# Optimization experiments

Measured on AMD Instinct MI355X. Metric: run time of the kernel, lower is better.

Reference implementation:

```python
import jax, jax.numpy as jnp
import numpy as np

NN = 262144        # total nodes = 4096 graphs * 64 nodes
EN = 524288        # directed edges
IN_DIM = 32
H = 128
PROP_STEPS = 3


def setup_inputs() -> dict:
    key = jax.random.key(0)
    ks = jax.random.split(key, 16)
    s = lambda d: 1.0 / np.sqrt(d)
    x = jax.random.normal(ks[0], (NN, IN_DIM), dtype=jnp.float32)
    # edges: random within each 64-node graph block would be most faithful; random
    # over NN is the same access pattern workload-wise. Use per-graph-local edges.
    src = jax.random.randint(ks[1], (EN,), 0, NN, dtype=jnp.int64)
    dst = jax.random.randint(ks[2], (EN,), 0, NN, dtype=jnp.int64)
    edge_index = jnp.stack([src, dst], axis=0)
    return {
        "x": x,
        "edge_index": edge_index,
        "W_in": jax.random.normal(ks[3], (IN_DIM, H), jnp.float32) * s(IN_DIM),
        "b_in": jnp.zeros((H,), jnp.float32),
        "W_e1": jax.random.normal(ks[4], (H, H), jnp.float32) * s(H),
        "b_e1": jnp.zeros((H,), jnp.float32),
        "W_e2": jax.random.normal(ks[5], (H, H), jnp.float32) * s(H),
        "b_e2": jnp.zeros((H,), jnp.float32),
        "W_ih": jax.random.normal(ks[6], (H, 3 * H), jnp.float32) * s(H),
        "b_ih": jnp.zeros((3 * H,), jnp.float32),
        "W_hh": jax.random.normal(ks[7], (H, 3 * H), jnp.float32) * s(H),
        "b_hh": jnp.zeros((3 * H,), jnp.float32),
        "W_out": jax.random.normal(ks[8], (H, 1), jnp.float32) * s(H),
        "b_out": jnp.zeros((1,), jnp.float32),
    }


def reference(x, edge_index, W_in, b_in, W_e1, b_e1, W_e2, b_e2,
              W_ih, b_ih, W_hh, b_hh, W_out, b_out):
    in_node, out_node = edge_index[0], edge_index[1]
    nn = x.shape[0]
    # input MLP: Linear + tanh
    h = jnp.tanh(x @ W_in + b_in)                         # [NN, H]
    for _ in range(PROP_STEPS):
        # unified edge MLP (hidden tanh + linear out), applied per node then gathered
        m = jnp.tanh(h @ W_e1 + b_e1) @ W_e2 + b_e2       # [NN, H]
        msg = m[in_node]                                  # [EN, H] gather
        ssum = jax.ops.segment_sum(msg, out_node, num_segments=nn)
        cnt = jax.ops.segment_sum(jnp.ones((msg.shape[0],), msg.dtype),
                                  out_node, num_segments=nn)
        m_agg = ssum / jnp.maximum(cnt, 1.0)[:, None]     # scatter_mean, [NN, H]
        # GRU cell update: input = m_agg, hidden = h (torch GRUCell math)
        gi = m_agg @ W_ih + b_ih                          # [NN, 3H]
        gh = h @ W_hh + b_hh                              # [NN, 3H]
        i_r, i_z, i_n = jnp.split(gi, 3, axis=-1)
        h_r, h_z, h_n = jnp.split(gh, 3, axis=-1)
        r = jax.nn.sigmoid(i_r + h_r)
        z = jax.nn.sigmoid(i_z + h_z)
        n = jnp.tanh(i_n + r * h_n)
        h = (1.0 - z) * n + z * h
    # unified output head: single Linear
    return h @ W_out + b_out                              # [NN, 1]
```

## Files before the change

kernel.cpp:

```cpp
#include <hip/hip_runtime.h>

#define NN 262144
#define EN 524288
#define HD 128
#define IND 32

#define NT64  (NN/64)
#define GRID_E 768
#define NT128 (NN/128)
#define GRID_G 256

typedef __attribute__((ext_vector_type(8))) short s16x8;
typedef __attribute__((ext_vector_type(4))) float f32x4;
typedef unsigned short u16;
typedef unsigned int u32;

#define MFMA(a,b,c) __builtin_amdgcn_mfma_f32_16x16x32_bf16(a,b,c,0,0,0)
#define SWZ(p) ((p) ^ ((((p)>>8)&7)<<4))

typedef __attribute__((address_space(1))) void gas_void;
typedef __attribute__((address_space(3))) void las_void;
__device__ __forceinline__ void gload16(const void* g, void* l){
  __builtin_amdgcn_global_load_lds((gas_void*)g, (las_void*)l, 16, 0, 0);
}

__device__ __forceinline__ u16 f2b(float f){
  u32 u = __builtin_bit_cast(u32, f);
  u = (u + 0x7fffu + ((u >> 16) & 1u)) >> 16;
  return (u16)u;
}
__device__ __forceinline__ float b2f(u32 lo16){ return __builtin_bit_cast(float, lo16 << 16); }
__device__ __forceinline__ float rcpf_(float x){ return __builtin_amdgcn_rcpf(x); }
__device__ __forceinline__ float fsig(float x){ return rcpf_(1.f + __expf(-x)); }
__device__ __forceinline__ float ftanh(float x){ return 1.f - 2.f*rcpf_(1.f + __expf(2.f*x)); }

__global__ __launch_bounds__(256) void k_w2bt(const float* __restrict__ W, u16* __restrict__ Wt, int K, int N){
  int idx = blockIdx.x*256 + threadIdx.x;
  if (idx >= K*N) return;
  int n = idx / K, k = idx - n*K;
  Wt[idx] = f2b(W[k*N + n]);
}

__global__ void k_eflag(const int* __restrict__ ei, int* __restrict__ flag){
  int v = ei[threadIdx.x*2 + 1];
  unsigned long long b = __ballot(v != 0);
  if (threadIdx.x == 0) flag[0] = (b == 0ULL) ? 1 : 0;
}
__device__ __forceinline__ int eget(const int* ei, int f, int which, int e){
  return f ? ei[(which*EN + e)*2] : ei[which*EN + e];
}

__global__ __launch_bounds__(256) void k_count(const int* __restrict__ ei, const int* __restrict__ flag, int* __restrict__ cnt){
  int e = blockIdx.x*256 + threadIdx.x;
  if (e < EN) atomicAdd(&cnt[eget(ei, flag[0], 1, e)], 1);
}
__global__ __launch_bounds__(256) void k_scan1(const int* __restrict__ cnt, int* __restrict__ excl, int* __restrict__ bsum){
  __shared__ int ws[4];
  int i = blockIdx.x*256 + threadIdx.x;
  int v = cnt[i];
  int ln = threadIdx.x & 63;
  int x = v;
  #pragma unroll
  for (int d=1; d<64; d<<=1){ int y = __shfl_up(x, d); if (ln >= d) x += y; }
  if (ln == 63) ws[threadIdx.x>>6] = x;
  __syncthreads();
  int wpre = 0;
  for (int j=0; j<(threadIdx.x>>6); ++j) wpre += ws[j];
  excl[i] = wpre + x - v;
  if (threadIdx.x == 255) bsum[blockIdx.x] = wpre + x;
}
__global__ __launch_bounds__(1024) void k_scan2(int* __restrict__ bsum){
  __shared__ int ws[16];
  int i = threadIdx.x;
  int v = bsum[i];
  int ln = i & 63;
  int x = v;
  #pragma unroll
  for (int d=1; d<64; d<<=1){ int y = __shfl_up(x, d); if (ln >= d) x += y; }
  if (ln == 63) ws[i>>6] = x;
  __syncthreads();
  int wpre = 0;
  for (int j=0; j<(i>>6); ++j) wpre += ws[j];
  bsum[i] = wpre + x - v;
}
__global__ __launch_bounds__(256) void k_scan3(const int* __restrict__ excl, const int* __restrict__ bsum, int* __restrict__ rp, int* __restrict__ cur){
  int i = blockIdx.x*256 + threadIdx.x;
  int v = excl[i] + bsum[blockIdx.x];
  rp[i] = v; cur[i] = v;
  if (i == 0) rp[NN] = EN;
}
__global__ __launch_bounds__(256) void k_fill(const int* __restrict__ ei, const int* __restrict__ flag, int* __restrict__ cur, int* __restrict__ cx){
  int e = blockIdx.x*256 + threadIdx.x;
  if (e >= EN) return;
  int f = flag[0];
  int p = atomicAdd(&cur[eget(ei, f, 1, e)], 1);
  cx[p] = eget(ei, f, 0, e);
}

__global__ __launch_bounds__(256) void k_input(const float* __restrict__ x, const u16* __restrict__ wt, const float* __restrict__ bias, u16* __restrict__ h){
  const int wv = threadIdx.x >> 6, ln = threadIdx.x & 63;
  const int l15 = ln & 15, lg = ln >> 4;
  const int base = blockIdx.x*128 + wv*32;
  s16x8 a[2];
  #pragma unroll
  for (int rt=0; rt<2; ++rt){
    const float* xp = x + (base + rt*16 + l15)*IND + lg*8;
    float4 v0 = *reinterpret_cast<const float4*>(xp);
    float4 v1 = *reinterpret_cast<const float4*>(xp + 4);
    s16x8 t;
    t[0]=(short)f2b(v0.x); t[1]=(short)f2b(v0.y); t[2]=(short)f2b(v0.z); t[3]=(short)f2b(v0.w);
    t[4]=(short)f2b(v1.x); t[5]=(short)f2b(v1.y); t[6]=(short)f2b(v1.z); t[7]=(short)f2b(v1.w);
    a[rt] = t;
  }
  #pragma unroll
  for (int cg=0; cg<8; ++cg){
    const int col = cg*16 + l15;
    s16x8 bf = *reinterpret_cast<const s16x8*>(wt + col*IND + lg*8);
    float bb = bias[col];
    f32x4 acc0 = {bb,bb,bb,bb}, acc1 = {bb,bb,bb,bb};
    acc0 = MFMA(a[0], bf, acc0);
    acc1 = MFMA(a[1], bf, acc1);
    #pragma unroll
    for (int r=0; r<4; ++r){
      h[(base + lg*4 + r)*HD + col]      = f2b(ftanh(acc0[r]));
      h[(base + 16 + lg*4 + r)*HD + col] = f2b(ftanh(acc1[r]));
    }
  }
}

__global__ __launch_bounds__(512) void k_edge(const u16* __restrict__ h, const u16* __restrict__ wt1, const float* __restrict__ b1,
                                              const u16* __restrict__ wt2, const float* __restrict__ b2, u16* __restrict__ m){
  extern __shared__ __align__(1024) unsigned char lds[];
  const int tid = threadIdx.x, wv = tid >> 6, ln = tid & 63;
  const int l15 = ln & 15, lg = ln >> 4;
  const int col = wv*16 + l15;

  s16x8 B1[4], B2[4];
  #pragma unroll
  for (int kk=0; kk<4; ++kk){
    const int ko = kk*32 + lg*8;
    B1[kk] = *reinterpret_cast<const s16x8*>(wt1 + (size_t)col*HD + ko);
    B2[kk] = *reinterpret_cast<const s16x8*>(wt2 + (size_t)col*HD + ko);
  }
  const float b1s = b1[col], b2s = b2[col];

  {
    const unsigned char* hg = (const unsigned char*)h + (size_t)blockIdx.x*64*256;
    #pragma unroll
    for (int i=0; i<2; ++i){
      int c = wv*2 + i;
      int p = c*1024 + ln*16;
      gload16(hg + SWZ(p), lds + c*1024);
    }
  }
  __syncthreads();

  unsigned char* tl = lds + 32768;
  int t = 0;
  #pragma unroll 1
  for (int tt = blockIdx.x; tt < NT64; tt += GRID_E, ++t){
    if (tt + GRID_E < NT64){
      const unsigned char* hg = (const unsigned char*)h + (size_t)(tt+GRID_E)*64*256;
      unsigned char* dst = lds + ((t+1)&1)*16384;
      #pragma unroll
      for (int i=0; i<2; ++i){
        int c = wv*2 + i;
        int p = c*1024 + ln*16;
        gload16(hg + SWZ(p), dst + c*1024);
      }
    }
    const unsigned char* hl = lds + (t&1)*16384;
    for (int rt=0; rt<4; ++rt){
      s16x8 a[4];
      #pragma unroll
      for (int kk=0; kk<4; ++kk){
        int row = rt*16 + l15;
        int p = row*256 + (((kk*4+lg) ^ (row&7))<<4);
        a[kk] = *reinterpret_cast<const s16x8*>(hl + p);
      }
      f32x4 acc = {b1s,b1s,b1s,b1s};
      __builtin_amdgcn_s_setprio(1);
      #pragma unroll
      for (int kk=0; kk<4; ++kk) acc = MFMA(a[kk], B1[kk], acc);
      __builtin_amdgcn_s_setprio(0);
      #pragma unroll
      for (int r=0; r<4; ++r){
        int row = rt*16 + lg*4 + r;
        int tb = row*256 + ((((col*2)>>4) ^ (row&7))<<4) + ((col&7)*2);
        *reinterpret_cast<u16*>(tl + tb) = f2b(ftanh(acc[r]));
      }
    }
    __syncthreads();
    for (int rt=0; rt<4; ++rt){
      s16x8 a[4];
      #pragma unroll
      for (int kk=0; kk<4; ++kk){
        int row = rt*16 + l15;
        int p = row*256 + (((kk*4+lg) ^ (row&7))<<4);
        a[kk] = *reinterpret_cast<const s16x8*>(tl + p);
      }
      f32x4 acc = {b2s,b2s,b2s,b2s};
      __builtin_amdgcn_s_setprio(1);
      #pragma unroll
      for (int kk=0; kk<4; ++kk) acc = MFMA(a[kk], B2[kk], acc);
      __builtin_amdgcn_s_setprio(0);
      #pragma unroll
      for (int r=0; r<4; ++r){
        int row = rt*16 + lg*4 + r;
        m[(size_t)(tt*64+row)*HD + col] = f2b(acc[r]);
      }
    }
    __syncthreads();
  }
}

__global__ __launch_bounds__(256) void k_agg(const u16* __restrict__ m, const int* __restrict__ rp, const int* __restrict__ cx, u16* __restrict__ magg){
  const int sub = threadIdx.x >> 5, l32 = threadIdx.x & 31;
  const int n = blockIdx.x*8 + sub;
  int s0 = rp[n], s1 = rp[n+1];
  float a0=0.f, a1=0.f, a2=0.f, a3=0.f;
  int p = s0;
  for (; p + 2 <= s1; p += 2){
    int na = cx[p], nb = cx[p+1];
    uint2 va = *reinterpret_cast<const uint2*>(m + (size_t)na*HD + l32*4);
    uint2 vb = *reinterpret_cast<const uint2*>(m + (size_t)nb*HD + l32*4);
    a0 += b2f(va.x & 0xffffu) + b2f(vb.x & 0xffffu);
    a1 += b2f(va.x >> 16)     + b2f(vb.x >> 16);
    a2 += b2f(va.y & 0xffffu) + b2f(vb.y & 0xffffu);
    a3 += b2f(va.y >> 16)     + b2f(vb.y >> 16);
  }
  if (p < s1){
    int na = cx[p];
    uint2 va = *reinterpret_cast<const uint2*>(m + (size_t)na*HD + l32*4);
    a0 += b2f(va.x & 0xffffu); a1 += b2f(va.x >> 16);
    a2 += b2f(va.y & 0xffffu); a3 += b2f(va.y >> 16);
  }
  int deg = s1 - s0;
  float inv = rcpf_((float)(deg > 0 ? deg : 1));
  uint2 o;
  o.x = (u32)f2b(a0*inv) | ((u32)f2b(a1*inv) << 16);
  o.y = (u32)f2b(a2*inv) | ((u32)f2b(a3*inv) << 16);
  *reinterpret_cast<uint2*>(magg + (size_t)n*HD + l32*4) = o;
}

__global__ __launch_bounds__(512) void k_gru(const u16* __restrict__ magg, u16* __restrict__ h,
    const u16* __restrict__ wtih, const float* __restrict__ bih,
    const u16* __restrict__ wthh, const float* __restrict__ bhh){
  extern __shared__ __align__(1024) unsigned char lds[];
  const int tid = threadIdx.x, wv = tid >> 6, ln = tid & 63;
  const int l15 = ln & 15, lg = ln >> 4;
  const int col = wv*16 + l15;
  const int ce = col & ~1;

  s16x8 B[6][4];
  #pragma unroll
  for (int kk=0; kk<4; ++kk){
    const int ko = kk*32 + lg*8;
    B[0][kk] = *reinterpret_cast<const s16x8*>(wtih + (size_t)(col       )*HD + ko);
    B[1][kk] = *reinterpret_cast<const s16x8*>(wtih + (size_t)(col +   HD)*HD + ko);
    B[2][kk] = *reinterpret_cast<const s16x8*>(wtih + (size_t)(col + 2*HD)*HD + ko);
    B[3][kk] = *reinterpret_cast<const s16x8*>(wthh + (size_t)(col       )*HD + ko);
    B[4][kk] = *reinterpret_cast<const s16x8*>(wthh + (size_t)(col +   HD)*HD + ko);
    B[5][kk] = *reinterpret_cast<const s16x8*>(wthh + (size_t)(col + 2*HD)*HD + ko);
  }
  const float brz = bih[col] + bhh[col];
  const float bzz = bih[col+HD] + bhh[col+HD];
  const float bin_ = bih[col+2*HD], bhn_ = bhh[col+2*HD];

  {
    const unsigned char* mg = (const unsigned char*)magg + (size_t)blockIdx.x*128*256;
    const unsigned char* hg = (const unsigned char*)h    + (size_t)blockIdx.x*128*256;
    #pragma unroll
    for (int i=0; i<8; ++i){
      int c = wv*8 + i;
      int p = (c & 31)*1024 + ln*16;
      gload16((c < 32 ? mg : hg) + SWZ(p), lds + c*1024);
    }
  }
  __syncthreads();

#define LOADA(rt, amg, ahh, hld) { \
    const int row_ = (rt)*16 + l15; \
    _Pragma("unroll") \
    for (int kk=0; kk<4; ++kk){ \
      int p_ = row_*256 + (((kk*4+lg) ^ (row_&7))<<4); \
      amg[kk] = *reinterpret_cast<const s16x8*>(mgl + p_); \
      ahh[kk] = *reinterpret_cast<const s16x8*>(hl + p_); } \
    _Pragma("unroll") \
    for (int r_=0; r_<4; ++r_){ \
      int hrow_ = (rt)*16 + lg*4 + r_; \
      int hb_ = hrow_*256 + ((((ce*2)>>4) ^ (hrow_&7))<<4) + ((ce&7)*2); \
      hld[r_] = *reinterpret_cast<const u32*>(hl + hb_); } }

#define MFMAS(amg, ahh, aR, aZ, aN, aH) { \
    aR = (f32x4){brz,brz,brz,brz}; aZ = (f32x4){bzz,bzz,bzz,bzz}; \
    aN = (f32x4){bin_,bin_,bin_,bin_}; aH = (f32x4){bhn_,bhn_,bhn_,bhn_}; \
    __builtin_amdgcn_s_setprio(1); \
    _Pragma("unroll") \
    for (int kk=0; kk<4; ++kk){ \
      aR = MFMA(amg[kk], B[0][kk], aR); \
      aZ = MFMA(amg[kk], B[1][kk], aZ); \
      aN = MFMA(amg[kk], B[2][kk], aN); \
      aH = MFMA(ahh[kk], B[5][kk], aH); \
      aR = MFMA(ahh[kk], B[3][kk], aR); \
      aZ = MFMA(ahh[kk], B[4][kk], aZ); } \
    __builtin_amdgcn_s_setprio(0); }

#define EPI(rt, aR, aZ, aN, aH, hld) { \
    _Pragma("unroll") \
    for (int r_=0; r_<4; ++r_){ \
      int row_ = (rt)*16 + lg*4 + r_; \
      float hold_ = __builtin_bit_cast(float, (col&1) ? (hld[r_] & 0xffff0000u) : (hld[r_] << 16)); \
      float rg_ = fsig(aR[r_]); \
      float zg_ = fsig(aZ[r_]); \
      float ng_ = ftanh(aN[r_] + rg_*aH[r_]); \
      h[(size_t)(tt*128+row_)*HD + col] = f2b(ng_ + zg_*(hold_ - ng_)); } }

  int t = 0;
  #pragma unroll 1
  for (int tt = blockIdx.x; tt < NT128; tt += GRID_G, ++t){
    if (tt + GRID_G < NT128){
      const unsigned char* mg = (const unsigned char*)magg + (size_t)(tt+GRID_G)*128*256;
      const unsigned char* hg = (const unsigned char*)h    + (size_t)(tt+GRID_G)*128*256;
      unsigned char* dst = lds + ((t+1)&1)*65536;
      #pragma unroll
      for (int i=0; i<8; ++i){
        int c = wv*8 + i;
        int p = (c & 31)*1024 + ln*16;
        gload16((c < 32 ? mg : hg) + SWZ(p), dst + c*1024);
      }
    }
    const unsigned char* mgl = lds + (t&1)*65536;
    const unsigned char* hl  = mgl + 32768;

    s16x8 amgA[4], ahhA[4], amgB[4], ahhB[4];
    u32 hldA[4], hldB[4];
    f32x4 rA, zA, nA, hA, rB, zB, nB, hB;

    LOADA(0, amgA, ahhA, hldA); MFMAS(amgA, ahhA, rA, zA, nA, hA);
    LOADA(1, amgB, ahhB, hldB); MFMAS(amgB, ahhB, rB, zB, nB, hB); EPI(0, rA, zA, nA, hA, hldA);
    LOADA(2, amgA, ahhA, hldA); MFMAS(amgA, ahhA, rA, zA, nA, hA); EPI(1, rB, zB, nB, hB, hldB);
    LOADA(3, amgB, ahhB, hldB); MFMAS(amgB, ahhB, rB, zB, nB, hB); EPI(2, rA, zA, nA, hA, hldA);
    LOADA(4, amgA, ahhA, hldA); MFMAS(amgA, ahhA, rA, zA, nA, hA); EPI(3, rB, zB, nB, hB, hldB);
    LOADA(5, amgB, ahhB, hldB); MFMAS(amgB, ahhB, rB, zB, nB, hB); EPI(4, rA, zA, nA, hA, hldA);
    LOADA(6, amgA, ahhA, hldA); MFMAS(amgA, ahhA, rA, zA, nA, hA); EPI(5, rB, zB, nB, hB, hldB);
    LOADA(7, amgB, ahhB, hldB); MFMAS(amgB, ahhB, rB, zB, nB, hB); EPI(6, rA, zA, nA, hA, hldA);
    EPI(7, rB, zB, nB, hB, hldB);

    __syncthreads();
  }
#undef LOADA
#undef MFMAS
#undef EPI
}

__global__ __launch_bounds__(256) void k_out(const u16* __restrict__ h, const float* __restrict__ wo, const float* __restrict__ bo, float* __restrict__ out){
  const int wv = threadIdx.x >> 6, ln = threadIdx.x & 63;
  const int n = (blockIdx.x*4 + wv)*4 + (ln >> 4);
  const int kc = (ln & 15)*8;
  uint4 v = *reinterpret_cast<const uint4*>(h + n*HD + kc);
  float4 w0 = *reinterpret_cast<const float4*>(wo + kc);
  float4 w1 = *reinterpret_cast<const float4*>(wo + kc + 4);
  float s = b2f(v.x & 0xffffu)*w0.x + b2f(v.x >> 16)*w0.y + b2f(v.y & 0xffffu)*w0.z + b2f(v.y >> 16)*w0.w
          + b2f(v.z & 0xffffu)*w1.x + b2f(v.z >> 16)*w1.y + b2f(v.w & 0xffffu)*w1.z + b2f(v.w >> 16)*w1.w;
  #pragma unroll
  for (int d=1; d<16; d<<=1) s += __shfl_xor(s, d, 16);
  if ((ln & 15) == 0) out[n] = s + bo[0];
}

#define AL256(x) ((((size_t)(x)) + 255) & ~(size_t)255)
static const size_t SZ_STATE = (size_t)NN*HD*2;
static const size_t OFF_H    = 0;
static const size_t OFF_M    = OFF_H + SZ_STATE;
static const size_t OFF_MAGG = OFF_M + SZ_STATE;
static const size_t OFF_RP   = OFF_MAGG + SZ_STATE;
static const size_t OFF_CUR  = OFF_RP + AL256((size_t)(NN+1)*4);
static const size_t OFF_CNT  = OFF_CUR + (size_t)NN*4;
static const size_t OFF_EXCL = OFF_CNT + (size_t)NN*4;
static const size_t OFF_BSUM = OFF_EXCL + (size_t)NN*4;
static const size_t OFF_CX   = OFF_BSUM + AL256(1024*4);
static const size_t OFF_FLAG = OFF_CX + (size_t)EN*4;
static const size_t OFF_WTIN = OFF_FLAG + 256;
static const size_t OFF_WTE1 = OFF_WTIN + AL256((size_t)IND*HD*2);
static const size_t OFF_WTE2 = OFF_WTE1 + AL256((size_t)HD*HD*2);
static const size_t OFF_WTIH = OFF_WTE2 + AL256((size_t)HD*HD*2);
static const size_t OFF_WTHH = OFF_WTIH + AL256((size_t)HD*3*HD*2);

extern "C" void kernel_launch(void* const* d_in, const int* in_sizes, int n_in,
                              void* d_out, int out_size, void* d_ws, size_t ws_size,
                              hipStream_t stream){
  const float* x    = (const float*)d_in[0];
  const int*   ei   = (const int*)d_in[1];
  const float* W_in = (const float*)d_in[2];  const float* b_in = (const float*)d_in[3];
  const float* W_e1 = (const float*)d_in[4];  const float* b_e1 = (const float*)d_in[5];
  const float* W_e2 = (const float*)d_in[6];  const float* b_e2 = (const float*)d_in[7];
  const float* W_ih = (const float*)d_in[8];  const float* b_ih = (const float*)d_in[9];
  const float* W_hh = (const float*)d_in[10]; const float* b_hh = (const float*)d_in[11];
  const float* W_out= (const float*)d_in[12]; const float* b_out= (const float*)d_in[13];
  float* out = (float*)d_out;

  char* ws = (char*)d_ws;
  u16* h    = (u16*)(ws + OFF_H);
  u16* m    = (u16*)(ws + OFF_M);
  u16* magg = (u16*)(ws + OFF_MAGG);
  int* rp   = (int*)(ws + OFF_RP);
  int* cur  = (int*)(ws + OFF_CUR);
  int* cnt  = (int*)(ws + OFF_CNT);
  int* excl = (int*)(ws + OFF_EXCL);
  int* bsum = (int*)(ws + OFF_BSUM);
  int* cx   = (int*)(ws + OFF_CX);
  int* flag = (int*)(ws + OFF_FLAG);
  u16* wtin = (u16*)(ws + OFF_WTIN);
  u16* wte1 = (u16*)(ws + OFF_WTE1);
  u16* wte2 = (u16*)(ws + OFF_WTE2);
  u16* wtih = (u16*)(ws + OFF_WTIH);
  u16* wthh = (u16*)(ws + OFF_WTHH);

  hipFuncSetAttribute((const void*)k_edge, hipFuncAttributeMaxDynamicSharedMemorySize, 49152);
  hipFuncSetAttribute((const void*)k_gru,  hipFuncAttributeMaxDynamicSharedMemorySize, 131072);

  hipMemsetAsync(cnt, 0, (size_t)NN*4, stream);

  k_w2bt<<<(IND*HD + 255)/256, 256, 0, stream>>>(W_in, wtin, IND, HD);
  k_w2bt<<<(HD*HD + 255)/256, 256, 0, stream>>>(W_e1, wte1, HD, HD);
  k_w2bt<<<(HD*HD + 255)/256, 256, 0, stream>>>(W_e2, wte2, HD, HD);
  k_w2bt<<<(HD*3*HD + 255)/256, 256, 0, stream>>>(W_ih, wtih, HD, 3*HD);
  k_w2bt<<<(HD*3*HD + 255)/256, 256, 0, stream>>>(W_hh, wthh, HD, 3*HD);

  k_eflag<<<1, 64, 0, stream>>>(ei, flag);
  k_count<<<EN/256, 256, 0, stream>>>(ei, flag, cnt);
  k_scan1<<<NN/256, 256, 0, stream>>>(cnt, excl, bsum);
  k_scan2<<<1, 1024, 0, stream>>>(bsum);
  k_scan3<<<NN/256, 256, 0, stream>>>(excl, bsum, rp, cur);
  k_fill<<<EN/256, 256, 0, stream>>>(ei, flag, cur, cx);

  k_input<<<NN/128, 256, 0, stream>>>(x, wtin, b_in, h);

  for (int it=0; it<3; ++it){
    k_edge<<<GRID_E, 512, 49152, stream>>>(h, wte1, b_e1, wte2, b_e2, m);
    k_agg<<<NN/8, 256, 0, stream>>>(m, rp, cx, magg);
    k_gru<<<GRID_G, 512, 131072, stream>>>(magg, h, wtih, b_ih, wthh, b_hh);
  }
  k_out<<<NN/16, 256, 0, stream>>>(h, W_out, b_out, out);
}
```

Baseline: 534.4 us.

## Split GRU tiles into column halves with ping-pong hidden-state buffers

The GRU kernel moves from 512-thread blocks over 128-row tiles to 256-thread blocks, two per CU, each handling 64 rows and half of the output columns. This halves LDS use per block and gives finer-grained work distribution. Because two blocks now read the same rows of h, the hidden state is ping-ponged between two buffers, and the message buffer reuses the output slot. The cost is that each block loads the full magg and h rows, so input traffic into LDS doubles. Activations also switch to exp2-based forms with fma, and stores use precomputed pointers.

```diff
diff --git a/kernel.cpp b/kernel.cpp
--- a/kernel.cpp
+++ b/kernel.cpp
@@ -7,8 +7,8 @@
 
 #define NT64  (NN/64)
 #define GRID_E 768
-#define NT128 (NN/128)
-#define GRID_G 256
+#define NJOB  (NT64*2)
+#define GRID_G2 512
 
 typedef __attribute__((ext_vector_type(8))) short s16x8;
 typedef __attribute__((ext_vector_type(4))) float f32x4;
@@ -29,10 +29,14 @@
   u = (u + 0x7fffu + ((u >> 16) & 1u)) >> 16;
   return (u16)u;
 }
+__device__ __forceinline__ u32 cvtpk(float lo, float hi){
+  return (u32)f2b(lo) | ((u32)f2b(hi) << 16);
+}
 __device__ __forceinline__ float b2f(u32 lo16){ return __builtin_bit_cast(float, lo16 << 16); }
 __device__ __forceinline__ float rcpf_(float x){ return __builtin_amdgcn_rcpf(x); }
-__device__ __forceinline__ float fsig(float x){ return rcpf_(1.f + __expf(-x)); }
-__device__ __forceinline__ float ftanh(float x){ return 1.f - 2.f*rcpf_(1.f + __expf(2.f*x)); }
+__device__ __forceinline__ float exp2_(float x){ return __builtin_amdgcn_exp2f(x); }
+__device__ __forceinline__ float fsig(float x){ return rcpf_(1.f + exp2_(x * -1.442695041f)); }
+__device__ __forceinline__ float ftanh(float x){ return fmaf(-2.f, rcpf_(1.f + exp2_(x * 2.885390082f)), 1.f); }
 
 __global__ __launch_bounds__(256) void k_w2bt(const float* __restrict__ W, u16* __restrict__ Wt, int K, int N){
   int idx = blockIdx.x*256 + threadIdx.x;
@@ -122,8 +126,8 @@
     acc1 = MFMA(a[1], bf, acc1);
     #pragma unroll
     for (int r=0; r<4; ++r){
-      h[(base + lg*4 + r)*HD + col]      = f2b(ftanh(acc0[r]));
-      h[(base + 16 + lg*4 + r)*HD + col] = f2b(ftanh(acc1[r]));
+      h[(size_t)(base + lg*4 + r)*HD + col]      = f2b(ftanh(acc0[r]));
+      h[(size_t)(base + 16 + lg*4 + r)*HD + col] = f2b(ftanh(acc1[r]));
     }
   }
 }
@@ -204,11 +208,11 @@
       #pragma unroll
       for (int kk=0; kk<4; ++kk) acc = MFMA(a[kk], B2[kk], acc);
       __builtin_amdgcn_s_setprio(0);
-      #pragma unroll
-      for (int r=0; r<4; ++r){
-        int row = rt*16 + lg*4 + r;
-        m[(size_t)(tt*64+row)*HD + col] = f2b(acc[r]);
-      }
+      u16* mp = m + (size_t)(tt*64 + rt*16 + lg*4)*HD + col;
+      mp[0]    = f2b(acc[0]);
+      mp[HD]   = f2b(acc[1]);
+      mp[2*HD] = f2b(acc[2]);
+      mp[3*HD] = f2b(acc[3]);
     }
     __syncthreads();
   }
@@ -238,18 +242,19 @@
   int deg = s1 - s0;
   float inv = rcpf_((float)(deg > 0 ? deg : 1));
   uint2 o;
-  o.x = (u32)f2b(a0*inv) | ((u32)f2b(a1*inv) << 16);
-  o.y = (u32)f2b(a2*inv) | ((u32)f2b(a3*inv) << 16);
+  o.x = cvtpk(a0*inv, a1*inv);
+  o.y = cvtpk(a2*inv, a3*inv);
   *reinterpret_cast<uint2*>(magg + (size_t)n*HD + l32*4) = o;
 }
 
-__global__ __launch_bounds__(512) void k_gru(const u16* __restrict__ magg, u16* __restrict__ h,
+__global__ __launch_bounds__(256, 2) void k_gru(const u16* __restrict__ magg, const u16* __restrict__ hin, u16* __restrict__ hout,
     const u16* __restrict__ wtih, const float* __restrict__ bih,
     const u16* __restrict__ wthh, const float* __restrict__ bhh){
   extern __shared__ __align__(1024) unsigned char lds[];
   const int tid = threadIdx.x, wv = tid >> 6, ln = tid & 63;
   const int l15 = ln & 15, lg = ln >> 4;
-  const int col = wv*16 + l15;
+  const int ch = blockIdx.x & 1;
+  const int col = ch*64 + wv*16 + l15;
   const int ce = col & ~1;
 
   s16x8 B[6][4];
@@ -268,13 +273,14 @@
   const float bin_ = bih[col+2*HD], bhn_ = bhh[col+2*HD];
 
   {
-    const unsigned char* mg = (const unsigned char*)magg + (size_t)blockIdx.x*128*256;
-    const unsigned char* hg = (const unsigned char*)h    + (size_t)blockIdx.x*128*256;
+    const size_t rbase = (size_t)(blockIdx.x >> 1)*64*256;
+    const unsigned char* mg = (const unsigned char*)magg + rbase;
+    const unsigned char* hg = (const unsigned char*)hin  + rbase;
     #pragma unroll
     for (int i=0; i<8; ++i){
       int c = wv*8 + i;
-      int p = (c & 31)*1024 + ln*16;
-      gload16((c < 32 ? mg : hg) + SWZ(p), lds + c*1024);
+      int p = (c & 15)*1024 + ln*16;
+      gload16((c < 16 ? mg : hg) + SWZ(p), lds + c*1024);
     }
   }
   __syncthreads();
@@ -307,31 +313,33 @@
     __builtin_amdgcn_s_setprio(0); }
 
 #define EPI(rt, aR, aZ, aN, aH, hld) { \
+    u16* hp_ = hout + (size_t)(rowt*64 + (rt)*16 + lg*4)*HD + col; \
     _Pragma("unroll") \
     for (int r_=0; r_<4; ++r_){ \
-      int row_ = (rt)*16 + lg*4 + r_; \
       float hold_ = __builtin_bit_cast(float, (col&1) ? (hld[r_] & 0xffff0000u) : (hld[r_] << 16)); \
       float rg_ = fsig(aR[r_]); \
       float zg_ = fsig(aZ[r_]); \
       float ng_ = ftanh(aN[r_] + rg_*aH[r_]); \
-      h[(size_t)(tt*128+row_)*HD + col] = f2b(ng_ + zg_*(hold_ - ng_)); } }
+      hp_[r_*HD] = f2b(ng_ + zg_*(hold_ - ng_)); } }
 
   int t = 0;
   #pragma unroll 1
-  for (int tt = blockIdx.x; tt < NT128; tt += GRID_G, ++t){
-    if (tt + GRID_G < NT128){
-      const unsigned char* mg = (const unsigned char*)magg + (size_t)(tt+GRID_G)*128*256;
-      const unsigned char* hg = (const unsigned char*)h    + (size_t)(tt+GRID_G)*128*256;
-      unsigned char* dst = lds + ((t+1)&1)*65536;
+  for (int job = blockIdx.x; job < NJOB; job += GRID_G2, ++t){
+    const int rowt = job >> 1;
+    if (job + GRID_G2 < NJOB){
+      const size_t rbase = (size_t)((job + GRID_G2) >> 1)*64*256;
+      const unsigned char* mg = (const unsigned char*)magg + rbase;
+      const unsigned char* hg = (const unsigned char*)hin  + rbase;
+      unsigned char* dst = lds + ((t+1)&1)*32768;
       #pragma unroll
       for (int i=0; i<8; ++i){
         int c = wv*8 + i;
-        int p = (c & 31)*1024 + ln*16;
-        gload16((c < 32 ? mg : hg) + SWZ(p), dst + c*1024);
+        int p = (c & 15)*1024 + ln*16;
+        gload16((c < 16 ? mg : hg) + SWZ(p), dst + c*1024);
       }
     }
-    const unsigned char* mgl = lds + (t&1)*65536;
-    const unsigned char* hl  = mgl + 32768;
+    const unsigned char* mgl = lds + (t&1)*32768;
+    const unsigned char* hl  = mgl + 16384;
 
     s16x8 amgA[4], ahhA[4], amgB[4], ahhB[4];
     u32 hldA[4], hldB[4];
@@ -341,11 +349,7 @@
     LOADA(1, amgB, ahhB, hldB); MFMAS(amgB, ahhB, rB, zB, nB, hB); EPI(0, rA, zA, nA, hA, hldA);
     LOADA(2, amgA, ahhA, hldA); MFMAS(amgA, ahhA, rA, zA, nA, hA); EPI(1, rB, zB, nB, hB, hldB);
     LOADA(3, amgB, ahhB, hldB); MFMAS(amgB, ahhB, rB, zB, nB, hB); EPI(2, rA, zA, nA, hA, hldA);
-    LOADA(4, amgA, ahhA, hldA); MFMAS(amgA, ahhA, rA, zA, nA, hA); EPI(3, rB, zB, nB, hB, hldB);
-    LOADA(5, amgB, ahhB, hldB); MFMAS(amgB, ahhB, rB, zB, nB, hB); EPI(4, rA, zA, nA, hA, hldA);
-    LOADA(6, amgA, ahhA, hldA); MFMAS(amgA, ahhA, rA, zA, nA, hA); EPI(5, rB, zB, nB, hB, hldB);
-    LOADA(7, amgB, ahhB, hldB); MFMAS(amgB, ahhB, rB, zB, nB, hB); EPI(6, rA, zA, nA, hA, hldA);
-    EPI(7, rB, zB, nB, hB, hldB);
+    EPI(3, rB, zB, nB, hB, hldB);
 
     __syncthreads();
   }
@@ -358,7 +362,7 @@
   const int wv = threadIdx.x >> 6, ln = threadIdx.x & 63;
   const int n = (blockIdx.x*4 + wv)*4 + (ln >> 4);
   const int kc = (ln & 15)*8;
-  uint4 v = *reinterpret_cast<const uint4*>(h + n*HD + kc);
+  uint4 v = *reinterpret_cast<const uint4*>(h + (size_t)n*HD + kc);
   float4 w0 = *reinterpret_cast<const float4*>(wo + kc);
   float4 w1 = *reinterpret_cast<const float4*>(wo + kc + 4);
   float s = b2f(v.x & 0xffffu)*w0.x + b2f(v.x >> 16)*w0.y + b2f(v.y & 0xffffu)*w0.z + b2f(v.y >> 16)*w0.w
@@ -370,9 +374,9 @@
 
 #define AL256(x) ((((size_t)(x)) + 255) & ~(size_t)255)
 static const size_t SZ_STATE = (size_t)NN*HD*2;
-static const size_t OFF_H    = 0;
-static const size_t OFF_M    = OFF_H + SZ_STATE;
-static const size_t OFF_MAGG = OFF_M + SZ_STATE;
+static const size_t OFF_HA   = 0;
+static const size_t OFF_HB   = OFF_HA + SZ_STATE;
+static const size_t OFF_MAGG = OFF_HB + SZ_STATE;
 static const size_t OFF_RP   = OFF_MAGG + SZ_STATE;
 static const size_t OFF_CUR  = OFF_RP + AL256((size_t)(NN+1)*4);
 static const size_t OFF_CNT  = OFF_CUR + (size_t)NN*4;
@@ -400,8 +404,8 @@
   float* out = (float*)d_out;
 
   char* ws = (char*)d_ws;
-  u16* h    = (u16*)(ws + OFF_H);
-  u16* m    = (u16*)(ws + OFF_M);
+  u16* hA   = (u16*)(ws + OFF_HA);
+  u16* hB   = (u16*)(ws + OFF_HB);
   u16* magg = (u16*)(ws + OFF_MAGG);
   int* rp   = (int*)(ws + OFF_RP);
   int* cur  = (int*)(ws + OFF_CUR);
@@ -417,7 +421,7 @@
   u16* wthh = (u16*)(ws + OFF_WTHH);
 
   hipFuncSetAttribute((const void*)k_edge, hipFuncAttributeMaxDynamicSharedMemorySize, 49152);
-  hipFuncSetAttribute((const void*)k_gru,  hipFuncAttributeMaxDynamicSharedMemorySize, 131072);
+  hipFuncSetAttribute((const void*)k_gru,  hipFuncAttributeMaxDynamicSharedMemorySize, 65536);
 
   hipMemsetAsync(cnt, 0, (size_t)NN*4, stream);
 
@@ -434,12 +438,14 @@
   k_scan3<<<NN/256, 256, 0, stream>>>(excl, bsum, rp, cur);
   k_fill<<<EN/256, 256, 0, stream>>>(ei, flag, cur, cx);
 
-  k_input<<<NN/128, 256, 0, stream>>>(x, wtin, b_in, h);
+  k_input<<<NN/128, 256, 0, stream>>>(x, wtin, b_in, hA);
 
   for (int it=0; it<3; ++it){
-    k_edge<<<GRID_E, 512, 49152, stream>>>(h, wte1, b_e1, wte2, b_e2, m);
-    k_agg<<<NN/8, 256, 0, stream>>>(m, rp, cx, magg);
-    k_gru<<<GRID_G, 512, 131072, stream>>>(magg, h, wtih, b_ih, wthh, b_hh);
-  }
-  k_out<<<NN/16, 256, 0, stream>>>(h, W_out, b_out, out);
-}
+    u16* hin  = (it & 1) ? hB : hA;
+    u16* hout = (it & 1) ? hA : hB;
+    k_edge<<<GRID_E, 512, 49152, stream>>>(hin, wte1, b_e1, wte2, b_e2, hout);
+    k_agg<<<NN/8, 256, 0, stream>>>(hout, rp, cx, magg);
+    k_gru<<<GRID_G2, 256, 65536, stream>>>(magg, hin, hout, wtih, b_ih, wthh, b_hh);
+  }
+  k_out<<<NN/16, 256, 0, stream>>>(hB, W_out, b_out, out);
+}
```

Result: no change. 527.3 us (-1.3%).
